# Optimization experiments

Measured on AMD Instinct MI355X. Metric: run time of the kernel, lower is better.

## Reference

```python
import jax, jax.numpy as jnp
import numpy as np

EMBED_DIM = 1024
NUM_HEADS = 16
HEAD_DIM = EMBED_DIM // NUM_HEADS
T, B = 2048, 2


def setup_inputs() -> dict:
    key = jax.random.key(0)
    ks = jax.random.split(key, 12)
    s = 1.0 / np.sqrt(EMBED_DIM)
    x = jax.random.normal(ks[0], (T, B, EMBED_DIM), dtype=jnp.float32)
    time_decay = jax.random.uniform(ks[1], (T, B, 1), dtype=jnp.float32)
    # causal mask: masked_fill where mask == 0
    attn_mask = jnp.tril(jnp.ones((T, T), dtype=jnp.int32))
    Wq = jax.random.uniform(ks[2], (EMBED_DIM, EMBED_DIM), jnp.float32, -s, s)
    bq = jax.random.uniform(ks[3], (EMBED_DIM,), jnp.float32, -s, s)
    Wk = jax.random.uniform(ks[4], (EMBED_DIM, EMBED_DIM), jnp.float32, -s, s)
    bk = jax.random.uniform(ks[5], (EMBED_DIM,), jnp.float32, -s, s)
    Wv = jax.random.uniform(ks[6], (EMBED_DIM, EMBED_DIM), jnp.float32, -s, s)
    bv = jax.random.uniform(ks[7], (EMBED_DIM,), jnp.float32, -s, s)
    Wo = jax.random.uniform(ks[8], (EMBED_DIM, EMBED_DIM), jnp.float32, -s, s)
    bo = jax.random.uniform(ks[9], (EMBED_DIM,), jnp.float32, -s, s)
    return {"x": x, "time_decay": time_decay, "attn_mask": attn_mask,
            "Wq": Wq, "bq": bq, "Wk": Wk, "bk": bk,
            "Wv": Wv, "bv": bv, "Wo": Wo, "bo": bo}


def reference(x, time_decay, attn_mask, Wq, bq, Wk, bk, Wv, bv, Wo, bo):
    t, b, e = x.shape
    h, d = NUM_HEADS, HEAD_DIM
    # linear (torch: y = x @ W.T + b), then split heads -> (B, H, T, D)
    def proj(W, bias):
        y = jnp.einsum('tbe,fe->tbf', x, W) + bias
        return y.reshape(t, b, h, d).transpose(1, 2, 0, 3)
    Q, K, V = proj(Wq, bq), proj(Wk, bk), proj(Wv, bv)
    scores = jnp.einsum('bhqd,bhkd->bhqk', Q, K) / np.sqrt(d).astype(jnp.float32)
    scores = jnp.where(attn_mask == 0, jnp.float32(-1e9), scores)
    attn = jax.nn.softmax(scores, axis=-1)
    out = jnp.einsum('bhqk,bhkd->bhqd', attn, V)      # (B,H,T,D)
    out = out.transpose(2, 0, 1, 3).reshape(t, b, e)   # (T,B,E)
    out = jnp.einsum('tbe,fe->tbf', out, Wo) + bo
    return out * time_decay
```

## Files before the change

### kernel.cpp

```cpp
#include <hip/hip_runtime.h>


typedef unsigned short u16;
typedef unsigned int u32;
typedef __attribute__((ext_vector_type(8))) short bf16x8_t;
typedef __attribute__((ext_vector_type(4))) float fx4_t;

#define T_SEQ 2048
#define BATCH 2
#define EMB   1024
#define NH    16
#define HD    64
#define MROWS (T_SEQ * BATCH)

#define EXP2F(x) __builtin_amdgcn_exp2f(x)

__device__ __forceinline__ float bf2f(u16 u) {
  union { unsigned int i; float f; } v;
  v.i = ((unsigned int)u) << 16;
  return v.f;
}
__device__ __forceinline__ u16 f2bf(float f) {
  union { float f; unsigned int i; } v;
  v.f = f;
  unsigned int x = v.i;
  unsigned int r = (x + 0x7fffu + ((x >> 16) & 1u)) >> 16;
  return (u16)r;
}
__device__ __forceinline__ u32 fbits(float f) {
  union { float f; u32 i; } v; v.f = f; return v.i;
}

__device__ __forceinline__ void glds16(const void* g, void* l) {
  __builtin_amdgcn_global_load_lds(
      (const __attribute__((address_space(1))) unsigned int*)g,
      (__attribute__((address_space(3))) unsigned int*)l, 16, 0, 0);
}


__global__ void cvt_all(const float* __restrict__ x,
                        const float* __restrict__ wq, const float* __restrict__ wk,
                        const float* __restrict__ wv, const float* __restrict__ wo,
                        u16* __restrict__ xb,
                        u16* __restrict__ wqb, u16* __restrict__ wkb,
                        u16* __restrict__ wvb, u16* __restrict__ wob) {
  int i = blockIdx.x * blockDim.x + threadIdx.x;
  const float* src; u16* dst; int off;
  if (i < 1048576)      { src = x;  dst = xb;  off = i; }
  else if (i < 1310720) { src = wq; dst = wqb; off = i - 1048576; }
  else if (i < 1572864) { src = wk; dst = wkb; off = i - 1310720; }
  else if (i < 1835008) { src = wv; dst = wvb; off = i - 1572864; }
  else                  { src = wo; dst = wob; off = i - 1835008; }
  float4 v = ((const float4*)src)[off];
  ushort4 o;
  o.x = f2bf(v.x); o.y = f2bf(v.y); o.z = f2bf(v.z); o.w = f2bf(v.w);
  ((ushort4*)dst)[off] = o;
}

__global__ __launch_bounds__(256, 2) void gemm_qkv(
    const u16* __restrict__ xb,
    const u16* __restrict__ wq, const u16* __restrict__ wk, const u16* __restrict__ wv,
    const float* __restrict__ bq, const float* __restrict__ bk, const float* __restrict__ bv,
    u16* __restrict__ Qm, u16* __restrict__ Km, u16* __restrict__ VTg) {
  __shared__ short As[128 * 64];
  __shared__ short Bs[128 * 64];

  const int z = blockIdx.z;
  const u16* W = (z == 0) ? wq : (z == 1) ? wk : wv;
  const float* bias = (z == 0) ? bq : (z == 1) ? bk : bv;

  const int tid = threadIdx.x;
  const int bm = blockIdx.x, bn = blockIdx.y;
  const int lane = tid & 63, w = tid >> 6;
  const int wm = w >> 1, wn = w & 1;
  const int lr = lane & 15, quad = lane >> 4;
  const int r0 = lane >> 3;
  const int c8s = ((lane & 7) ^ r0) * 8;
  const int sw = (lr & 7);

  fx4_t acc[4][4];
#pragma unroll
  for (int i = 0; i < 4; i++)
#pragma unroll
    for (int j = 0; j < 4; j++) acc[i][j] = (fx4_t){0.f, 0.f, 0.f, 0.f};

  for (int k0 = 0; k0 < EMB; k0 += 64) {
#pragma unroll
    for (int i = 0; i < 4; i++) {
      const int rr = w * 32 + i * 8;
      const int ml = bm * 128 + rr + r0;
      const int grow = (z == 2) ? (((ml & 2047) << 1) | (ml >> 11)) : ml;
      glds16(xb + (size_t)grow * EMB + k0 + c8s, &As[rr * 64]);
      glds16(W + (size_t)(bn * 128 + rr + r0) * EMB + k0 + c8s, &Bs[rr * 64]);
    }
    __syncthreads();
#pragma unroll
    for (int ks = 0; ks < 2; ++ks) {
      bf16x8_t a[4], b[4];
#pragma unroll
      for (int i = 0; i < 4; i++)
        a[i] = *(const bf16x8_t*)&As[(wm * 64 + i * 16 + lr) * 64 + (((ks * 4 + quad) ^ sw) * 8)];
#pragma unroll
      for (int j = 0; j < 4; j++)
        b[j] = *(const bf16x8_t*)&Bs[(wn * 64 + j * 16 + lr) * 64 + (((ks * 4 + quad) ^ sw) * 8)];
      if (z == 2) {
#pragma unroll
        for (int i = 0; i < 4; i++)
#pragma unroll
          for (int j = 0; j < 4; j++)
            acc[i][j] = __builtin_amdgcn_mfma_f32_16x16x32_bf16(b[j], a[i], acc[i][j], 0, 0, 0);
      } else {
#pragma unroll
        for (int i = 0; i < 4; i++)
#pragma unroll
          for (int j = 0; j < 4; j++)
            acc[i][j] = __builtin_amdgcn_mfma_f32_16x16x32_bf16(a[i], b[j], acc[i][j], 0, 0, 0);
      }
    }
    __syncthreads();
  }

  if (z == 2) {
#pragma unroll
    for (int i = 0; i < 4; i++) {
#pragma unroll
      for (int j = 0; j < 4; j++) {
#pragma unroll
        for (int r = 0; r < 4; r++) {
          const int n = bn * 128 + wn * 64 + j * 16 + quad * 4 + r;
          const int ml = bm * 128 + wm * 64 + i * 16 + lr;
          const int t = ml & 2047, bb = ml >> 11;
          const int h = n >> 6, d = n & 63;
          VTg[((size_t)(bb * NH + h) * HD + d) * T_SEQ + t] = f2bf(acc[i][j][r] + bias[n]);
        }
      }
    }
  } else {
    u16* dst = (z == 0) ? Qm : Km;
#pragma unroll
    for (int i = 0; i < 4; i++) {
#pragma unroll
      for (int j = 0; j < 4; j++) {
        const int n = bn * 128 + wn * 64 + j * 16 + lr;
        const float bsv = bias[n];
#pragma unroll
        for (int r = 0; r < 4; r++) {
          const int m = bm * 128 + wm * 64 + i * 16 + quad * 4 + r;
          dst[(size_t)m * EMB + n] = f2bf(acc[i][j][r] + bsv);
        }
      }
    }
  }
}

__global__ __launch_bounds__(256, 2) void gemm_out(
    const u16* __restrict__ Ob, const u16* __restrict__ wo,
    const float* __restrict__ bo, const float* __restrict__ td,
    float* __restrict__ out) {
  __shared__ short As[64 * 64];
  __shared__ short Bs[128 * 64];

  const int tid = threadIdx.x;
  const int bm = blockIdx.x, bn = blockIdx.y;
  const int lane = tid & 63, w = tid >> 6;
  const int wm = w >> 1, wn = w & 1;
  const int lr = lane & 15, quad = lane >> 4;
  const int r0 = lane >> 3;
  const int c8s = ((lane & 7) ^ r0) * 8;
  const int sw = (lr & 7);

  fx4_t acc[2][4];
#pragma unroll
  for (int i = 0; i < 2; i++)
#pragma unroll
    for (int j = 0; j < 4; j++) acc[i][j] = (fx4_t){0.f, 0.f, 0.f, 0.f};

  for (int k0 = 0; k0 < EMB; k0 += 64) {
#pragma unroll
    for (int i = 0; i < 2; i++) {
      const int rr = w * 16 + i * 8;
      glds16(Ob + (size_t)(bm * 64 + rr + r0) * EMB + k0 + c8s, &As[rr * 64]);
    }
#pragma unroll
    for (int i = 0; i < 4; i++) {
      const int rr = w * 32 + i * 8;
      glds16(wo + (size_t)(bn * 128 + rr + r0) * EMB + k0 + c8s, &Bs[rr * 64]);
    }
    __syncthreads();
#pragma unroll
    for (int ks = 0; ks < 2; ++ks) {
      bf16x8_t a[2], b[4];
#pragma unroll
      for (int i = 0; i < 2; i++)
        a[i] = *(const bf16x8_t*)&As[(wm * 32 + i * 16 + lr) * 64 + (((ks * 4 + quad) ^ sw) * 8)];
#pragma unroll
      for (int j = 0; j < 4; j++)
        b[j] = *(const bf16x8_t*)&Bs[(wn * 64 + j * 16 + lr) * 64 + (((ks * 4 + quad) ^ sw) * 8)];
#pragma unroll
      for (int i = 0; i < 2; i++)
#pragma unroll
        for (int j = 0; j < 4; j++)
          acc[i][j] = __builtin_amdgcn_mfma_f32_16x16x32_bf16(a[i], b[j], acc[i][j], 0, 0, 0);
    }
    __syncthreads();
  }

#pragma unroll
  for (int i = 0; i < 2; i++) {
#pragma unroll
    for (int j = 0; j < 4; j++) {
      const int n = bn * 128 + wn * 64 + j * 16 + lr;
      const float bsv = bo[n];
#pragma unroll
      for (int r = 0; r < 4; r++) {
        const int m = bm * 64 + wm * 32 + i * 16 + quad * 4 + r;
        out[(size_t)m * EMB + n] = (acc[i][j][r] + bsv) * td[m];
      }
    }
  }
}

__global__ __launch_bounds__(256, 3) void attn_mfma8(
    const u16* __restrict__ Qm, const u16* __restrict__ Km, const u16* __restrict__ VTg,
    u16* __restrict__ Ob) {
  __shared__ short Kd[2][64 * 64];
  __shared__ short Vd[2][64 * 64];
  __shared__ short Ps[4][16 * 72];

  const int blk = blockIdx.x;
  const int bh = blk & 31;
  const int j = blk >> 5;
  const int qt = (j & 1) ? (31 - (j >> 1)) : (j >> 1);
  const int qb = qt * 64;
  const int b = bh >> 4, h = bh & 15;

  const int tid = threadIdx.x;
  const int w = tid >> 6, lane = tid & 63;
  const int lr = lane & 15, quad = lane >> 4;
  const int r0 = lane >> 3;
  const int c8s = ((lane & 7) ^ r0) * 8;
  const int sw = (lr & 7);

  const u16* Qbase = Qm + (size_t)b * EMB + (size_t)h * HD;
  const u16* Kbase = Km + (size_t)b * EMB + (size_t)h * HD;
  const u16* VTb = VTg + (size_t)bh * HD * T_SEQ;

  const float QSCALE = 0.18033688f;
  bf16x8_t qf[2];
#pragma unroll
  for (int ks = 0; ks < 2; ks++) {
    bf16x8_t v = *(const bf16x8_t*)(Qbase + (size_t)(qb + w * 16 + lr) * 2 * EMB + ks * 32 + quad * 8);
    bf16x8_t o;
#pragma unroll
    for (int e = 0; e < 8; e++) o[e] = (short)f2bf(bf2f((u16)v[e]) * QSCALE);
    qf[ks] = o;
  }

  fx4_t acc_o[4];
#pragma unroll
  for (int dn = 0; dn < 4; dn++) acc_o[dn] = (fx4_t){0.f, 0.f, 0.f, 0.f};
  float l_par = 0.f;

#define STAGE(kt_, buf_)                                                            \
  {                                                                                 \
    const int k0_ = (kt_) * 64;                                                     \
    _Pragma("unroll")                                                               \
    for (int i = 0; i < 2; i++) {                                                   \
      const int rr = w * 16 + i * 8;                                                \
      glds16(Kbase + (size_t)(k0_ + rr + r0) * 2 * EMB + c8s, &Kd[buf_][rr * 64]);  \
      glds16(VTb + (size_t)(rr + r0) * T_SEQ + k0_ + c8s, &Vd[buf_][rr * 64]);      \
    }                                                                               \
  }

  const int nkt = qt + 1;
  STAGE(0, 0);
  __syncthreads();

  for (int kt = 0; kt < nkt; kt++) {
    const int buf = kt & 1;
    if (kt + 1 < nkt) STAGE(kt + 1, buf ^ 1);

    fx4_t st[4];
#pragma unroll
    for (int nt = 0; nt < 4; nt++) st[nt] = (fx4_t){0.f, 0.f, 0.f, 0.f};
#pragma unroll
    for (int ks = 0; ks < 2; ks++) {
#pragma unroll
      for (int nt = 0; nt < 4; nt++) {
        bf16x8_t kf = *(const bf16x8_t*)&Kd[buf][(nt * 16 + lr) * 64 + (((ks * 4 + quad) ^ sw) * 8)];
        st[nt] = __builtin_amdgcn_mfma_f32_16x16x32_bf16(kf, qf[ks], st[nt], 0, 0, 0);
      }
    }

    bf16x8_t vf[2][4];
#pragma unroll
    for (int ks = 0; ks < 2; ks++)
#pragma unroll
      for (int dn = 0; dn < 4; dn++)
        vf[ks][dn] = *(const bf16x8_t*)&Vd[buf][(dn * 16 + lr) * 64 + (((ks * 4 + quad) ^ sw) * 8)];

    if (kt == qt) {
#pragma unroll
      for (int nt = 0; nt < 4; nt++)
#pragma unroll
        for (int r = 0; r < 4; r++)
          if (nt * 16 + quad * 4 + r > w * 16 + lr) st[nt][r] = -1e30f;
    }

    short* Pw = Ps[w];
#pragma unroll
    for (int nt = 0; nt < 4; nt++) {
      float e0 = EXP2F(st[nt][0]);
      float e1 = EXP2F(st[nt][1]);
      float e2 = EXP2F(st[nt][2]);
      float e3 = EXP2F(st[nt][3]);
      u32 p01 = (fbits(e0) >> 16) | (fbits(e1) & 0xFFFF0000u);
      u32 p23 = (fbits(e2) >> 16) | (fbits(e3) & 0xFFFF0000u);
      uint2 pv; pv.x = p01; pv.y = p23;
      *(uint2*)&Pw[lr * 72 + nt * 16 + quad * 4] = pv;
      l_par += (e0 + e1) + (e2 + e3);
    }

#pragma unroll
    for (int ks = 0; ks < 2; ks++) {
      bf16x8_t pf = *(const bf16x8_t*)&Pw[lr * 72 + ks * 32 + quad * 8];
#pragma unroll
      for (int dn = 0; dn < 4; dn++)
        acc_o[dn] = __builtin_amdgcn_mfma_f32_16x16x32_bf16(pf, vf[ks][dn], acc_o[dn], 0, 0, 0);
    }

    __syncthreads();
  }
#undef STAGE

  l_par += __shfl_xor(l_par, 16);
  l_par += __shfl_xor(l_par, 32);
  const float inv = 1.0f / l_par;
#pragma unroll
  for (int r = 0; r < 4; r++) {
    const float inv_r = __shfl(inv, quad * 4 + r);
    const int t = qb + w * 16 + quad * 4 + r;
#pragma unroll
    for (int dn = 0; dn < 4; dn++) {
      const int d = dn * 16 + lr;
      Ob[(size_t)(t * BATCH + b) * EMB + h * HD + d] = f2bf(acc_o[dn][r] * inv_r);
    }
  }
}

extern "C" void kernel_launch(void* const* d_in, const int* in_sizes, int n_in,
                              void* d_out, int out_size, void* d_ws, size_t ws_size,
                              hipStream_t stream) {
  const float* x  = (const float*)d_in[0];
  const float* td = (const float*)d_in[1];
  const float* Wq = (const float*)d_in[3];
  const float* bq = (const float*)d_in[4];
  const float* Wk = (const float*)d_in[5];
  const float* bk = (const float*)d_in[6];
  const float* Wv = (const float*)d_in[7];
  const float* bv = (const float*)d_in[8];
  const float* Wo = (const float*)d_in[9];
  const float* bo = (const float*)d_in[10];
  float* out = (float*)d_out;

  char* ws = (char*)d_ws;
  u16* xb  = (u16*)(ws + 0);
  u16* wqb = (u16*)(ws + ((size_t)8  << 20));
  u16* wkb = (u16*)(ws + ((size_t)10 << 20));
  u16* wvb = (u16*)(ws + ((size_t)12 << 20));
  u16* wob = (u16*)(ws + ((size_t)14 << 20));
  u16* Qm  = (u16*)(ws + ((size_t)16 << 20));
  u16* Km  = (u16*)(ws + ((size_t)24 << 20));
  u16* VTg = (u16*)(ws + ((size_t)32 << 20));
  u16* Ob  = xb;

  cvt_all<<<8192, 256, 0, stream>>>(x, Wq, Wk, Wv, Wo, xb, wqb, wkb, wvb, wob);

  gemm_qkv<<<dim3(MROWS / 128, EMB / 128, 3), 256, 0, stream>>>(
      xb, wqb, wkb, wvb, bq, bk, bv, Qm, Km, VTg);

  attn_mfma8<<<1024, 256, 0, stream>>>(Qm, Km, VTg, Ob);

  gemm_out<<<dim3(MROWS / 64, EMB / 128), 256, 0, stream>>>(Ob, wob, bo, td, out);
}
```

Before: 192.8 us.

## Rewrite QKV GEMM with 256x256 tiles, 8 waves and double-buffered LDS

```diff
diff --git a/kernel.cpp b/kernel.cpp
--- a/kernel.cpp
+++ b/kernel.cpp
@@ -57,13 +57,13 @@
   ((ushort4*)dst)[off] = o;
 }
 
-__global__ __launch_bounds__(256, 2) void gemm_qkv(
+__global__ __launch_bounds__(512, 2) void gemm_qkv8(
     const u16* __restrict__ xb,
     const u16* __restrict__ wq, const u16* __restrict__ wk, const u16* __restrict__ wv,
     const float* __restrict__ bq, const float* __restrict__ bk, const float* __restrict__ bv,
     u16* __restrict__ Qm, u16* __restrict__ Km, u16* __restrict__ VTg) {
-  __shared__ short As[128 * 64];
-  __shared__ short Bs[128 * 64];
+  __shared__ short As[2][256 * 64];
+  __shared__ short Bs[2][256 * 64];
 
   const int z = blockIdx.z;
   const u16* W = (z == 0) ? wq : (z == 1) ? wk : wv;
@@ -72,81 +72,143 @@
   const int tid = threadIdx.x;
   const int bm = blockIdx.x, bn = blockIdx.y;
   const int lane = tid & 63, w = tid >> 6;
-  const int wm = w >> 1, wn = w & 1;
+  const int wm = w >> 2, wn = w & 3;
   const int lr = lane & 15, quad = lane >> 4;
   const int r0 = lane >> 3;
   const int c8s = ((lane & 7) ^ r0) * 8;
-  const int sw = (lr & 7);
-
-  fx4_t acc[4][4];
-#pragma unroll
-  for (int i = 0; i < 4; i++)
+  const int sw = lr & 7;
+
+  fx4_t acc[8][4];
+#pragma unroll
+  for (int i = 0; i < 8; i++)
 #pragma unroll
     for (int j = 0; j < 4; j++) acc[i][j] = (fx4_t){0.f, 0.f, 0.f, 0.f};
 
-  for (int k0 = 0; k0 < EMB; k0 += 64) {
-#pragma unroll
-    for (int i = 0; i < 4; i++) {
-      const int rr = w * 32 + i * 8;
-      const int ml = bm * 128 + rr + r0;
-      const int grow = (z == 2) ? (((ml & 2047) << 1) | (ml >> 11)) : ml;
-      glds16(xb + (size_t)grow * EMB + k0 + c8s, &As[rr * 64]);
-      glds16(W + (size_t)(bn * 128 + rr + r0) * EMB + k0 + c8s, &Bs[rr * 64]);
-    }
-    __syncthreads();
-#pragma unroll
-    for (int ks = 0; ks < 2; ++ks) {
-      bf16x8_t a[4], b[4];
-#pragma unroll
-      for (int i = 0; i < 4; i++)
-        a[i] = *(const bf16x8_t*)&As[(wm * 64 + i * 16 + lr) * 64 + (((ks * 4 + quad) ^ sw) * 8)];
-#pragma unroll
-      for (int j = 0; j < 4; j++)
-        b[j] = *(const bf16x8_t*)&Bs[(wn * 64 + j * 16 + lr) * 64 + (((ks * 4 + quad) ^ sw) * 8)];
-      if (z == 2) {
-#pragma unroll
-        for (int i = 0; i < 4; i++)
-#pragma unroll
-          for (int j = 0; j < 4; j++)
-            acc[i][j] = __builtin_amdgcn_mfma_f32_16x16x32_bf16(b[j], a[i], acc[i][j], 0, 0, 0);
-      } else {
-#pragma unroll
-        for (int i = 0; i < 4; i++)
-#pragma unroll
-          for (int j = 0; j < 4; j++)
-            acc[i][j] = __builtin_amdgcn_mfma_f32_16x16x32_bf16(a[i], b[j], acc[i][j], 0, 0, 0);
-      }
-    }
-    __syncthreads();
-  }
+  bf16x8_t afr[4][2], bfr[4][2];
+
+#define BAR() asm volatile("s_barrier" ::: "memory")
+
+#define STAGE_A(kt_, h_, bi_)                                                       \
+  {                                                                                 \
+    const int k0_ = (kt_) * 64;                                                     \
+    _Pragma("unroll")                                                               \
+    for (int rnd = 0; rnd < 2; rnd++) {                                             \
+      const int rowb = (h_) * 128 + rnd * 64 + w * 8;                               \
+      const int ml = bm * 256 + rowb + r0;                                          \
+      const int grow = (z == 2) ? (((ml & 2047) << 1) | (ml >> 11)) : ml;           \
+      glds16(xb + (size_t)grow * EMB + k0_ + c8s, &As[bi_][rowb * 64]);             \
+    }                                                                               \
+  }
+#define STAGE_B(kt_, h_, bi_)                                                       \
+  {                                                                                 \
+    const int k0_ = (kt_) * 64;                                                     \
+    _Pragma("unroll")                                                               \
+    for (int rnd = 0; rnd < 2; rnd++) {                                             \
+      const int rowb = (h_) * 128 + rnd * 64 + w * 8;                               \
+      glds16(W + (size_t)(bn * 256 + rowb + r0) * EMB + k0_ + c8s,                  \
+             &Bs[bi_][rowb * 64]);                                                  \
+    }                                                                               \
+  }
+
+#define READ_A(mh_, bi_)                                                            \
+  _Pragma("unroll")                                                                 \
+  for (int i = 0; i < 4; i++)                                                       \
+    _Pragma("unroll")                                                               \
+    for (int ks = 0; ks < 2; ks++)                                                  \
+      afr[i][ks] = *(const bf16x8_t*)&As[bi_][((mh_) * 128 + wm * 64 + i * 16 + lr) * 64 + \
+                                             (((ks * 4 + quad) ^ sw) * 8)];
+#define READ_B(nb_, bi_)                                                            \
+  _Pragma("unroll")                                                                 \
+  for (int j = 0; j < 2; j++)                                                       \
+    _Pragma("unroll")                                                               \
+    for (int ks = 0; ks < 2; ks++)                                                  \
+      bfr[(nb_) * 2 + j][ks] = *(const bf16x8_t*)&Bs[bi_][((nb_) * 128 + wn * 32 + j * 16 + lr) * 64 + \
+                                                          (((ks * 4 + quad) ^ sw) * 8)];
+
+#define MMA_Q(mh_, nb_)                                                             \
+  __builtin_amdgcn_s_setprio(1);                                                    \
+  _Pragma("unroll")                                                                 \
+  for (int ks = 0; ks < 2; ks++)                                                    \
+    _Pragma("unroll")                                                               \
+    for (int i = 0; i < 4; i++)                                                     \
+      _Pragma("unroll")                                                             \
+      for (int j = 0; j < 2; j++) {                                                 \
+        const int ig = (mh_) * 4 + i, jg = (nb_) * 2 + j;                           \
+        if (z == 2)                                                                 \
+          acc[ig][jg] = __builtin_amdgcn_mfma_f32_16x16x32_bf16(                    \
+              bfr[jg][ks], afr[i][ks], acc[ig][jg], 0, 0, 0);                       \
+        else                                                                        \
+          acc[ig][jg] = __builtin_amdgcn_mfma_f32_16x16x32_bf16(                    \
+              afr[i][ks], bfr[jg][ks], acc[ig][jg], 0, 0, 0);                       \
+      }                                                                             \
+  __builtin_amdgcn_s_setprio(0);
+
+  const int nkt = EMB / 64;
+
+  STAGE_A(0, 0, 0); STAGE_B(0, 0, 0); STAGE_B(0, 1, 0); STAGE_A(0, 1, 0);
+  STAGE_A(1, 0, 1); STAGE_B(1, 0, 1); STAGE_B(1, 1, 1);
+  asm volatile("s_waitcnt vmcnt(6)" ::: "memory");
+  BAR();
+
+  for (int t = 0; t < nkt; t++) {
+    const int buf = t & 1;
+    if (t + 1 < nkt) STAGE_A(t + 1, 1, buf ^ 1);
+    READ_A(0, buf); READ_B(0, buf);
+    BAR();
+    MMA_Q(0, 0);
+    BAR();
+    if (t + 2 < nkt) STAGE_A(t + 2, 0, buf);
+    READ_B(1, buf);
+    BAR();
+    MMA_Q(0, 1);
+    BAR();
+    if (t + 2 < nkt) STAGE_B(t + 2, 0, buf);
+    READ_A(1, buf);
+    BAR();
+    MMA_Q(1, 1);
+    BAR();
+    if (t + 2 < nkt) STAGE_B(t + 2, 1, buf);
+    BAR();
+    MMA_Q(1, 0);
+    if (t + 2 < nkt)      asm volatile("s_waitcnt vmcnt(6)" ::: "memory");
+    else if (t + 1 < nkt) asm volatile("s_waitcnt vmcnt(0)" ::: "memory");
+    BAR();
+  }
+#undef STAGE_A
+#undef STAGE_B
+#undef READ_A
+#undef READ_B
+#undef MMA_Q
+#undef BAR
 
   if (z == 2) {
 #pragma unroll
-    for (int i = 0; i < 4; i++) {
+    for (int ig = 0; ig < 8; ig++) {
 #pragma unroll
       for (int j = 0; j < 4; j++) {
+        const int nb = bn * 256 + (j >> 1) * 128 + wn * 32 + (j & 1) * 16;
+        const int ml = bm * 256 + (ig >> 2) * 128 + wm * 64 + (ig & 3) * 16 + lr;
+        const int t = ml & 2047, bb = ml >> 11;
 #pragma unroll
         for (int r = 0; r < 4; r++) {
-          const int n = bn * 128 + wn * 64 + j * 16 + quad * 4 + r;
-          const int ml = bm * 128 + wm * 64 + i * 16 + lr;
-          const int t = ml & 2047, bb = ml >> 11;
-          const int h = n >> 6, d = n & 63;
-          VTg[((size_t)(bb * NH + h) * HD + d) * T_SEQ + t] = f2bf(acc[i][j][r] + bias[n]);
+          const int n = nb + quad * 4 + r;
+          VTg[((size_t)(bb * NH + (n >> 6)) * HD + (n & 63)) * T_SEQ + t] =
+              f2bf(acc[ig][j][r] + bias[n]);
         }
       }
     }
   } else {
     u16* dst = (z == 0) ? Qm : Km;
 #pragma unroll
-    for (int i = 0; i < 4; i++) {
+    for (int ig = 0; ig < 8; ig++) {
 #pragma unroll
       for (int j = 0; j < 4; j++) {
-        const int n = bn * 128 + wn * 64 + j * 16 + lr;
+        const int n = bn * 256 + (j >> 1) * 128 + wn * 32 + (j & 1) * 16 + lr;
         const float bsv = bias[n];
 #pragma unroll
         for (int r = 0; r < 4; r++) {
-          const int m = bm * 128 + wm * 64 + i * 16 + quad * 4 + r;
-          dst[(size_t)m * EMB + n] = f2bf(acc[i][j][r] + bsv);
+          const int m = bm * 256 + (ig >> 2) * 128 + wm * 64 + (ig & 3) * 16 + quad * 4 + r;
+          dst[(size_t)m * EMB + n] = f2bf(acc[ig][j][r] + bsv);
         }
       }
     }
@@ -376,7 +438,7 @@
 
   cvt_all<<<8192, 256, 0, stream>>>(x, Wq, Wk, Wv, Wo, xb, wqb, wkb, wvb, wob);
 
-  gemm_qkv<<<dim3(MROWS / 128, EMB / 128, 3), 256, 0, stream>>>(
+  gemm_qkv8<<<dim3(MROWS / 256, EMB / 256, 3), 512, 0, stream>>>(
       xb, wqb, wkb, wvb, bq, bk, bv, Qm, Km, VTg);
 
   attn_mfma8<<<1024, 256, 0, stream>>>(Qm, Km, VTg, Ob);
```

Result: slower. 214.1 us (+11.1%).

## Double-buffer QKV GEMM loads and widen attention query tile to 128 rows

Applied to the files above, without the earlier changes.

```diff
diff --git a/kernel.cpp b/kernel.cpp
--- a/kernel.cpp
+++ b/kernel.cpp
@@ -62,8 +62,8 @@
     const u16* __restrict__ wq, const u16* __restrict__ wk, const u16* __restrict__ wv,
     const float* __restrict__ bq, const float* __restrict__ bk, const float* __restrict__ bv,
     u16* __restrict__ Qm, u16* __restrict__ Km, u16* __restrict__ VTg) {
-  __shared__ short As[128 * 64];
-  __shared__ short Bs[128 * 64];
+  __shared__ short As[2][128 * 64];
+  __shared__ short Bs[2][128 * 64];
 
   const int z = blockIdx.z;
   const u16* W = (z == 0) ? wq : (z == 1) ? wk : wv;
@@ -84,25 +84,36 @@
 #pragma unroll
     for (int j = 0; j < 4; j++) acc[i][j] = (fx4_t){0.f, 0.f, 0.f, 0.f};
 
-  for (int k0 = 0; k0 < EMB; k0 += 64) {
-#pragma unroll
-    for (int i = 0; i < 4; i++) {
-      const int rr = w * 32 + i * 8;
-      const int ml = bm * 128 + rr + r0;
-      const int grow = (z == 2) ? (((ml & 2047) << 1) | (ml >> 11)) : ml;
-      glds16(xb + (size_t)grow * EMB + k0 + c8s, &As[rr * 64]);
-      glds16(W + (size_t)(bn * 128 + rr + r0) * EMB + k0 + c8s, &Bs[rr * 64]);
-    }
-    __syncthreads();
+#define STAGE(kt_, bi_)                                                          \
+  {                                                                              \
+    const int k0_ = (kt_) * 64;                                                  \
+    _Pragma("unroll")                                                            \
+    for (int i = 0; i < 4; i++) {                                                \
+      const int rr = w * 32 + i * 8;                                             \
+      const int ml = bm * 128 + rr + r0;                                         \
+      const int grow = (z == 2) ? (((ml & 2047) << 1) | (ml >> 11)) : ml;        \
+      glds16(xb + (size_t)grow * EMB + k0_ + c8s, &As[bi_][rr * 64]);            \
+      glds16(W + (size_t)(bn * 128 + rr + r0) * EMB + k0_ + c8s,                 \
+             &Bs[bi_][rr * 64]);                                                 \
+    }                                                                            \
+  }
+
+  const int nkt = EMB / 64;
+  STAGE(0, 0);
+  __syncthreads();
+
+  for (int kt = 0; kt < nkt; kt++) {
+    const int buf = kt & 1;
+    if (kt + 1 < nkt) STAGE(kt + 1, buf ^ 1);
 #pragma unroll
     for (int ks = 0; ks < 2; ++ks) {
       bf16x8_t a[4], b[4];
 #pragma unroll
       for (int i = 0; i < 4; i++)
-        a[i] = *(const bf16x8_t*)&As[(wm * 64 + i * 16 + lr) * 64 + (((ks * 4 + quad) ^ sw) * 8)];
+        a[i] = *(const bf16x8_t*)&As[buf][(wm * 64 + i * 16 + lr) * 64 + (((ks * 4 + quad) ^ sw) * 8)];
 #pragma unroll
       for (int j = 0; j < 4; j++)
-        b[j] = *(const bf16x8_t*)&Bs[(wn * 64 + j * 16 + lr) * 64 + (((ks * 4 + quad) ^ sw) * 8)];
+        b[j] = *(const bf16x8_t*)&Bs[buf][(wn * 64 + j * 16 + lr) * 64 + (((ks * 4 + quad) ^ sw) * 8)];
       if (z == 2) {
 #pragma unroll
         for (int i = 0; i < 4; i++)
@@ -119,6 +130,7 @@
     }
     __syncthreads();
   }
+#undef STAGE
 
   if (z == 2) {
 #pragma unroll
@@ -220,18 +232,18 @@
   }
 }
 
-__global__ __launch_bounds__(256, 3) void attn_mfma8(
+__global__ __launch_bounds__(256, 2) void attn_mfma16(
     const u16* __restrict__ Qm, const u16* __restrict__ Km, const u16* __restrict__ VTg,
     u16* __restrict__ Ob) {
   __shared__ short Kd[2][64 * 64];
   __shared__ short Vd[2][64 * 64];
-  __shared__ short Ps[4][16 * 72];
+  __shared__ short Ps[4][32 * 72];
 
   const int blk = blockIdx.x;
   const int bh = blk & 31;
   const int j = blk >> 5;
-  const int qt = (j & 1) ? (31 - (j >> 1)) : (j >> 1);
-  const int qb = qt * 64;
+  const int qt = (j & 1) ? (15 - (j >> 1)) : (j >> 1);
+  const int qb = qt * 128;
   const int b = bh >> 4, h = bh & 15;
 
   const int tid = threadIdx.x;
@@ -246,20 +258,25 @@
   const u16* VTb = VTg + (size_t)bh * HD * T_SEQ;
 
   const float QSCALE = 0.18033688f;
-  bf16x8_t qf[2];
-#pragma unroll
-  for (int ks = 0; ks < 2; ks++) {
-    bf16x8_t v = *(const bf16x8_t*)(Qbase + (size_t)(qb + w * 16 + lr) * 2 * EMB + ks * 32 + quad * 8);
-    bf16x8_t o;
-#pragma unroll
-    for (int e = 0; e < 8; e++) o[e] = (short)f2bf(bf2f((u16)v[e]) * QSCALE);
-    qf[ks] = o;
-  }
-
-  fx4_t acc_o[4];
-#pragma unroll
-  for (int dn = 0; dn < 4; dn++) acc_o[dn] = (fx4_t){0.f, 0.f, 0.f, 0.f};
-  float l_par = 0.f;
+  bf16x8_t qf[2][2];
+#pragma unroll
+  for (int qi = 0; qi < 2; qi++)
+#pragma unroll
+    for (int ks = 0; ks < 2; ks++) {
+      bf16x8_t v = *(const bf16x8_t*)(Qbase +
+          (size_t)(qb + w * 32 + qi * 16 + lr) * 2 * EMB + ks * 32 + quad * 8);
+      bf16x8_t o;
+#pragma unroll
+      for (int e = 0; e < 8; e++) o[e] = (short)f2bf(bf2f((u16)v[e]) * QSCALE);
+      qf[qi][ks] = o;
+    }
+
+  fx4_t acc_o[2][4];
+#pragma unroll
+  for (int qi = 0; qi < 2; qi++)
+#pragma unroll
+    for (int dn = 0; dn < 4; dn++) acc_o[qi][dn] = (fx4_t){0.f, 0.f, 0.f, 0.f};
+  float l_par[2] = {0.f, 0.f};
 
 #define STAGE(kt_, buf_)                                                            \
   {                                                                                 \
@@ -272,7 +289,7 @@
     }                                                                               \
   }
 
-  const int nkt = qt + 1;
+  const int nkt = 2 * qt + 2;
   STAGE(0, 0);
   __syncthreads();
 
@@ -280,70 +297,89 @@
     const int buf = kt & 1;
     if (kt + 1 < nkt) STAGE(kt + 1, buf ^ 1);
 
-    fx4_t st[4];
-#pragma unroll
-    for (int nt = 0; nt < 4; nt++) st[nt] = (fx4_t){0.f, 0.f, 0.f, 0.f};
-#pragma unroll
-    for (int ks = 0; ks < 2; ks++) {
-#pragma unroll
-      for (int nt = 0; nt < 4; nt++) {
-        bf16x8_t kf = *(const bf16x8_t*)&Kd[buf][(nt * 16 + lr) * 64 + (((ks * 4 + quad) ^ sw) * 8)];
-        st[nt] = __builtin_amdgcn_mfma_f32_16x16x32_bf16(kf, qf[ks], st[nt], 0, 0, 0);
-      }
-    }
-
-    bf16x8_t vf[2][4];
-#pragma unroll
-    for (int ks = 0; ks < 2; ks++)
-#pragma unroll
-      for (int dn = 0; dn < 4; dn++)
-        vf[ks][dn] = *(const bf16x8_t*)&Vd[buf][(dn * 16 + lr) * 64 + (((ks * 4 + quad) ^ sw) * 8)];
-
-    if (kt == qt) {
-#pragma unroll
-      for (int nt = 0; nt < 4; nt++)
-#pragma unroll
-        for (int r = 0; r < 4; r++)
-          if (nt * 16 + quad * 4 + r > w * 16 + lr) st[nt][r] = -1e30f;
-    }
-
-    short* Pw = Ps[w];
-#pragma unroll
-    for (int nt = 0; nt < 4; nt++) {
-      float e0 = EXP2F(st[nt][0]);
-      float e1 = EXP2F(st[nt][1]);
-      float e2 = EXP2F(st[nt][2]);
-      float e3 = EXP2F(st[nt][3]);
-      u32 p01 = (fbits(e0) >> 16) | (fbits(e1) & 0xFFFF0000u);
-      u32 p23 = (fbits(e2) >> 16) | (fbits(e3) & 0xFFFF0000u);
-      uint2 pv; pv.x = p01; pv.y = p23;
-      *(uint2*)&Pw[lr * 72 + nt * 16 + quad * 4] = pv;
-      l_par += (e0 + e1) + (e2 + e3);
-    }
-
-#pragma unroll
-    for (int ks = 0; ks < 2; ks++) {
-      bf16x8_t pf = *(const bf16x8_t*)&Pw[lr * 72 + ks * 32 + quad * 8];
-#pragma unroll
-      for (int dn = 0; dn < 4; dn++)
-        acc_o[dn] = __builtin_amdgcn_mfma_f32_16x16x32_bf16(pf, vf[ks][dn], acc_o[dn], 0, 0, 0);
+    const int koff = kt * 64 - qb - w * 32;
+    if (koff < 32) {
+      fx4_t st[2][4];
+#pragma unroll
+      for (int qi = 0; qi < 2; qi++)
+#pragma unroll
+        for (int nt = 0; nt < 4; nt++) st[qi][nt] = (fx4_t){0.f, 0.f, 0.f, 0.f};
+#pragma unroll
+      for (int ks = 0; ks < 2; ks++) {
+#pragma unroll
+        for (int nt = 0; nt < 4; nt++) {
+          bf16x8_t kf = *(const bf16x8_t*)&Kd[buf][(nt * 16 + lr) * 64 + (((ks * 4 + quad) ^ sw) * 8)];
+#pragma unroll
+          for (int qi = 0; qi < 2; qi++)
+            st[qi][nt] = __builtin_amdgcn_mfma_f32_16x16x32_bf16(kf, qf[qi][ks], st[qi][nt], 0, 0, 0);
+        }
+      }
+
+      bf16x8_t vf[2][4];
+#pragma unroll
+      for (int ks = 0; ks < 2; ks++)
+#pragma unroll
+        for (int dn = 0; dn < 4; dn++)
+          vf[ks][dn] = *(const bf16x8_t*)&Vd[buf][(dn * 16 + lr) * 64 + (((ks * 4 + quad) ^ sw) * 8)];
+
+      if (koff > -64) {
+#pragma unroll
+        for (int qi = 0; qi < 2; qi++)
+#pragma unroll
+          for (int nt = 0; nt < 4; nt++)
+#pragma unroll
+            for (int r = 0; r < 4; r++)
+              if (koff + nt * 16 + quad * 4 + r > qi * 16 + lr) st[qi][nt][r] = -1e30f;
+      }
+
+      short* Pw = Ps[w];
+#pragma unroll
+      for (int qi = 0; qi < 2; qi++) {
+#pragma unroll
+        for (int nt = 0; nt < 4; nt++) {
+          float e0 = EXP2F(st[qi][nt][0]);
+          float e1 = EXP2F(st[qi][nt][1]);
+          float e2 = EXP2F(st[qi][nt][2]);
+          float e3 = EXP2F(st[qi][nt][3]);
+          u32 p01 = (fbits(e0) >> 16) | (fbits(e1) & 0xFFFF0000u);
+          u32 p23 = (fbits(e2) >> 16) | (fbits(e3) & 0xFFFF0000u);
+          uint2 pv; pv.x = p01; pv.y = p23;
+          *(uint2*)&Pw[(qi * 16 + lr) * 72 + nt * 16 + quad * 4] = pv;
+          l_par[qi] += (e0 + e1) + (e2 + e3);
+        }
+      }
+
+#pragma unroll
+      for (int qi = 0; qi < 2; qi++) {
+#pragma unroll
+        for (int ks = 0; ks < 2; ks++) {
+          bf16x8_t pf = *(const bf16x8_t*)&Pw[(qi * 16 + lr) * 72 + ks * 32 + quad * 8];
+#pragma unroll
+          for (int dn = 0; dn < 4; dn++)
+            acc_o[qi][dn] = __builtin_amdgcn_mfma_f32_16x16x32_bf16(pf, vf[ks][dn], acc_o[qi][dn], 0, 0, 0);
+        }
+      }
     }
 
     __syncthreads();
   }
 #undef STAGE
 
-  l_par += __shfl_xor(l_par, 16);
-  l_par += __shfl_xor(l_par, 32);
-  const float inv = 1.0f / l_par;
-#pragma unroll
-  for (int r = 0; r < 4; r++) {
-    const float inv_r = __shfl(inv, quad * 4 + r);
-    const int t = qb + w * 16 + quad * 4 + r;
-#pragma unroll
-    for (int dn = 0; dn < 4; dn++) {
-      const int d = dn * 16 + lr;
-      Ob[(size_t)(t * BATCH + b) * EMB + h * HD + d] = f2bf(acc_o[dn][r] * inv_r);
+#pragma unroll
+  for (int qi = 0; qi < 2; qi++) {
+    float lp = l_par[qi];
+    lp += __shfl_xor(lp, 16);
+    lp += __shfl_xor(lp, 32);
+    const float inv = 1.0f / lp;
+#pragma unroll
+    for (int r = 0; r < 4; r++) {
+      const float inv_r = __shfl(inv, quad * 4 + r);
+      const int t = qb + w * 32 + qi * 16 + quad * 4 + r;
+#pragma unroll
+      for (int dn = 0; dn < 4; dn++) {
+        const int d = dn * 16 + lr;
+        Ob[(size_t)(t * BATCH + b) * EMB + h * HD + d] = f2bf(acc_o[qi][dn][r] * inv_r);
+      }
     }
   }
 }
@@ -379,7 +415,7 @@
   gemm_qkv<<<dim3(MROWS / 128, EMB / 128, 3), 256, 0, stream>>>(
       xb, wqb, wkb, wvb, bq, bk, bv, Qm, Km, VTg);
 
-  attn_mfma8<<<1024, 256, 0, stream>>>(Qm, Km, VTg, Ob);
+  attn_mfma16<<<512, 256, 0, stream>>>(Qm, Km, VTg, Ob);
 
   gemm_out<<<dim3(MROWS / 64, EMB / 128), 256, 0, stream>>>(Ob, wob, bo, td, out);
 }
```

Measured after the change: 200.6 us. 4.0% more time.

## Double-buffer shared memory tiles in QKV projection GEMM

Applied to the files above, without the earlier changes.

```diff
diff --git a/kernel.cpp b/kernel.cpp
--- a/kernel.cpp
+++ b/kernel.cpp
@@ -62,8 +62,8 @@
     const u16* __restrict__ wq, const u16* __restrict__ wk, const u16* __restrict__ wv,
     const float* __restrict__ bq, const float* __restrict__ bk, const float* __restrict__ bv,
     u16* __restrict__ Qm, u16* __restrict__ Km, u16* __restrict__ VTg) {
-  __shared__ short As[128 * 64];
-  __shared__ short Bs[128 * 64];
+  __shared__ short As[2][128 * 64];
+  __shared__ short Bs[2][128 * 64];
 
   const int z = blockIdx.z;
   const u16* W = (z == 0) ? wq : (z == 1) ? wk : wv;
@@ -84,25 +84,36 @@
 #pragma unroll
     for (int j = 0; j < 4; j++) acc[i][j] = (fx4_t){0.f, 0.f, 0.f, 0.f};
 
-  for (int k0 = 0; k0 < EMB; k0 += 64) {
-#pragma unroll
-    for (int i = 0; i < 4; i++) {
-      const int rr = w * 32 + i * 8;
-      const int ml = bm * 128 + rr + r0;
-      const int grow = (z == 2) ? (((ml & 2047) << 1) | (ml >> 11)) : ml;
-      glds16(xb + (size_t)grow * EMB + k0 + c8s, &As[rr * 64]);
-      glds16(W + (size_t)(bn * 128 + rr + r0) * EMB + k0 + c8s, &Bs[rr * 64]);
-    }
-    __syncthreads();
+#define STAGE(kt_, bi_)                                                          \
+  {                                                                              \
+    const int k0_ = (kt_) * 64;                                                  \
+    _Pragma("unroll")                                                            \
+    for (int i = 0; i < 4; i++) {                                                \
+      const int rr = w * 32 + i * 8;                                             \
+      const int ml = bm * 128 + rr + r0;                                         \
+      const int grow = (z == 2) ? (((ml & 2047) << 1) | (ml >> 11)) : ml;        \
+      glds16(xb + (size_t)grow * EMB + k0_ + c8s, &As[bi_][rr * 64]);            \
+      glds16(W + (size_t)(bn * 128 + rr + r0) * EMB + k0_ + c8s,                 \
+             &Bs[bi_][rr * 64]);                                                 \
+    }                                                                            \
+  }
+
+  const int nkt = EMB / 64;
+  STAGE(0, 0);
+  __syncthreads();
+
+  for (int kt = 0; kt < nkt; kt++) {
+    const int buf = kt & 1;
+    if (kt + 1 < nkt) STAGE(kt + 1, buf ^ 1);
 #pragma unroll
     for (int ks = 0; ks < 2; ++ks) {
       bf16x8_t a[4], b[4];
 #pragma unroll
       for (int i = 0; i < 4; i++)
-        a[i] = *(const bf16x8_t*)&As[(wm * 64 + i * 16 + lr) * 64 + (((ks * 4 + quad) ^ sw) * 8)];
+        a[i] = *(const bf16x8_t*)&As[buf][(wm * 64 + i * 16 + lr) * 64 + (((ks * 4 + quad) ^ sw) * 8)];
 #pragma unroll
       for (int j = 0; j < 4; j++)
-        b[j] = *(const bf16x8_t*)&Bs[(wn * 64 + j * 16 + lr) * 64 + (((ks * 4 + quad) ^ sw) * 8)];
+        b[j] = *(const bf16x8_t*)&Bs[buf][(wn * 64 + j * 16 + lr) * 64 + (((ks * 4 + quad) ^ sw) * 8)];
       if (z == 2) {
 #pragma unroll
         for (int i = 0; i < 4; i++)
@@ -119,6 +130,7 @@
     }
     __syncthreads();
   }
+#undef STAGE
 
   if (z == 2) {
 #pragma unroll
```

After: 192.6 us. No clear change (-0.1%).
